# Kernel tuning notes

Hardware: AMD Instinct MI355X
Metric: run time of the kernel (lower is better)

## Reference

```python
import jax, jax.numpy as jnp
import numpy as np

B, T, D = 64, 2048, 256


def setup_inputs() -> dict:
    key = jax.random.key(0)
    k0, k1, k2, k3 = jax.random.split(key, 4)
    x0 = jax.random.normal(k0, (B, D), dtype=jnp.float32)
    I = jax.random.normal(k1, (B, T, D), dtype=jnp.float32)
    # Scale transition matrix so spectral norm < 1 (stable 2048-step recurrence),
    # mimicking eW = expm((W - I)*dt/tau) which is contractive for stable W.
    eW = jax.random.normal(k2, (D, D), dtype=jnp.float32) * (0.9 / np.sqrt(D))
    W_inv_eW = jax.random.normal(k3, (D, D), dtype=jnp.float32) * (1.0 / np.sqrt(D))
    return {"x0": x0, "I": I, "eW": eW, "W_inv_eW": W_inv_eW}


def reference(x0, I, eW, W_inv_eW):
    # x[:,0]=x0; x[:,t] = x[:,t-1] @ eW.T + I[:,t-1] @ W_inv_eW.T
    u = jnp.einsum('btd,sd->bts', I, W_inv_eW)  # [B, T, D], precompute input drive

    def step(x, u_t):
        x_new = x @ eW.T + u_t  # [B, D]
        return x_new, x_new

    # only u[:, :T-1] is consumed (x[:,t] uses I[:,t-1])
    _, xs = jax.lax.scan(step, x0, jnp.swapaxes(u[:, :-1], 0, 1))  # xs: [T-1, B, D]
    x = jnp.concatenate([x0[:, None, :], jnp.swapaxes(xs, 0, 1)], axis=1)  # [B, T, D]
    return x
```

## Files before the change

### kernel.cpp

```cpp
#include <hip/hip_runtime.h>
#include <stdint.h>
#include <stddef.h>


#define BATCH 64
#define TLEN 2048
#define DDIM 256
#define CHUNK 32
#define NCHUNK 64

typedef __attribute__((ext_vector_type(8))) short short8;
typedef __attribute__((ext_vector_type(4))) float f32x4;
typedef __attribute__((ext_vector_type(16))) float f32x16;

#define MFMA16(a, b, c) __builtin_amdgcn_mfma_f32_16x16x32_bf16((a), (b), (c), 0, 0, 0)
#define MFMA32(a, b, c) __builtin_amdgcn_mfma_f32_32x32x16_bf16((a), (b), (c), 0, 0, 0)
#define PIN8(x) asm volatile("" : "+v"(x))

__device__ __forceinline__ uint16_t f2bf(float f) {
  union { float f; uint32_t u; } v; v.f = f;
  return (uint16_t)((v.u + 0x7fffu + ((v.u >> 16) & 1u)) >> 16);
}
__device__ __forceinline__ float bf2f(uint16_t h) {
  union { uint32_t u; float f; } v; v.u = ((uint32_t)h) << 16;
  return v.f;
}

__device__ __forceinline__ void split8(const float* fv, short8& hi, short8& lo) {
#pragma unroll
  for (int j = 0; j < 8; ++j) {
    uint16_t hb = f2bf(fv[j]);
    hi[j] = (short)hb;
    lo[j] = (short)f2bf(fv[j] - bf2f(hb));
  }
}

__device__ __forceinline__ uint32_t swz(int row) {
  return ((uint32_t)((row & 7) << 4)) ^ ((uint32_t)(((row >> 3) & 1) << 7));
}
__device__ __forceinline__ uint32_t swz32(int row) {
  return ((uint32_t)((row & 7) << 4)) ^ ((uint32_t)(((row >> 3) & 3) << 7));
}

__device__ __forceinline__ void wg_barrier() {
  __builtin_amdgcn_sched_barrier(0);
  asm volatile("s_waitcnt lgkmcnt(0)" ::: "memory");
  __builtin_amdgcn_s_barrier();
  asm volatile("" ::: "memory");
  __builtin_amdgcn_sched_barrier(0);
}

#define WS_M1F    (0)
#define WS_M1_HI  (256 * 1024)
#define WS_M1_LO  (384 * 1024)
#define WS_M2F    (512 * 1024)
#define WS_M2_HI  (768 * 1024)
#define WS_M2_LO  (896 * 1024)
#define WS_M3F    (1024 * 1024)
#define WS_M3_HI  (1280 * 1024)
#define WS_M3_LO  (1408 * 1024)
#define WS_S      (2560 * 1024)

__global__ __launch_bounds__(512, 1) void k_u(const float* __restrict__ I,
                                              const float* __restrict__ Wi,
                                              float* __restrict__ out) {
  const int tid = threadIdx.x;
  const int w = tid >> 6, l = tid & 63, l31 = l & 31, half = l >> 5;
  const int ns = w * 32;
  __shared__ __align__(16) uint16_t sIh[2][8192];
  __shared__ __align__(16) uint16_t sIl[2][8192];

  short8 bh[16], bl[16];
#pragma unroll
  for (int ks = 0; ks < 16; ++ks) {
    const float* wp = Wi + (size_t)(ns + l31) * 256 + ks * 16 + half * 8;
    f32x4 f0 = *reinterpret_cast<const f32x4*>(wp);
    f32x4 f1 = *reinterpret_cast<const f32x4*>(wp + 4);
    float fv[8] = {f0[0], f0[1], f0[2], f0[3], f1[0], f1[1], f1[2], f1[3]};
    split8(fv, bh[ks], bl[ks]);
    PIN8(bh[ks]);
    PIN8(bl[ks]);
  }

  const int srow = tid >> 4;
  const int sc0 = (tid & 15) * 16;
  const uint32_t wb0 = ((uint32_t)(srow * 512 + sc0 * 2)) ^ swz32(srow);
  const uint32_t wb1 = ((uint32_t)(srow * 512 + sc0 * 2 + 16)) ^ swz32(srow);

  const int b0 = blockIdx.x >> 6;
  const int tt = blockIdx.x & 63;
  const bool edge = (tt == 63);
  const size_t S4 = (size_t)4 * TLEN * DDIM;
  const float* Ip = I + ((size_t)b0 * TLEN + tt * 32 + srow) * DDIM + sc0;
  float* Op = out + ((size_t)b0 * TLEN + tt * 32 + 1) * DDIM + ns + l31;

  uint32_t ro[16];
#pragma unroll
  for (int ks = 0; ks < 16; ++ks)
    ro[ks] = ((uint32_t)(l31 * 512 + ks * 32 + half * 16)) ^ swz32(l31);
  int rowoff[16];
#pragma unroll
  for (int r = 0; r < 16; ++r)
    rowoff[r] = ((r & 3) + 8 * (r >> 2) + 4 * half) * DDIM;

  f32x4 ra[4], rb[4];
  auto loadI = [&](int it, f32x4 (&dst)[4]) {
    const float* src = Ip + (size_t)it * S4;
#pragma unroll
    for (int j = 0; j < 4; ++j)
      dst[j] = *reinterpret_cast<const f32x4*>(src + j * 4);
  };

  auto do_tile = [&](int it, f32x4 (&cur)[4], int q, bool pre) {
    short8 hi[2], lo[2];
#pragma unroll
    for (int h2 = 0; h2 < 2; ++h2) {
      float fv[8] = {cur[h2 * 2][0], cur[h2 * 2][1], cur[h2 * 2][2], cur[h2 * 2][3],
                     cur[h2 * 2 + 1][0], cur[h2 * 2 + 1][1], cur[h2 * 2 + 1][2], cur[h2 * 2 + 1][3]};
      split8(fv, hi[h2], lo[h2]);
    }
    if (pre) loadI(it + 2, cur);
    *reinterpret_cast<short8*>(reinterpret_cast<char*>(sIh[q]) + wb0) = hi[0];
    *reinterpret_cast<short8*>(reinterpret_cast<char*>(sIh[q]) + wb1) = hi[1];
    *reinterpret_cast<short8*>(reinterpret_cast<char*>(sIl[q]) + wb0) = lo[0];
    *reinterpret_cast<short8*>(reinterpret_cast<char*>(sIl[q]) + wb1) = lo[1];
    wg_barrier();
    f32x16 acc;
#pragma unroll
    for (int j = 0; j < 16; ++j) acc[j] = 0.f;
    __builtin_amdgcn_s_setprio(1);
#pragma unroll
    for (int ks = 0; ks < 16; ++ks) {
      short8 ih = *reinterpret_cast<const short8*>((const char*)sIh[q] + ro[ks]);
      short8 il = *reinterpret_cast<const short8*>((const char*)sIl[q] + ro[ks]);
      acc = MFMA32(ih, bh[ks], acc);
      acc = MFMA32(il, bh[ks], acc);
      acc = MFMA32(ih, bl[ks], acc);
    }
    __builtin_amdgcn_s_setprio(0);
    float* ob = Op + (size_t)it * S4;
    if (!edge) {
#pragma unroll
      for (int r = 0; r < 16; ++r) ob[rowoff[r]] = acc[r];
    } else {
#pragma unroll
      for (int r = 0; r < 16; ++r)
        if (rowoff[r] < 31 * DDIM) ob[rowoff[r]] = acc[r];
    }
  };

  loadI(0, ra);
  loadI(1, rb);
#pragma unroll 1
  for (int it = 0; it < 16; it += 2) {
    do_tile(it, ra, 0, it + 2 < 16);
    do_tile(it + 1, rb, 1, it + 3 < 16);
  }
}

__global__ __launch_bounds__(1024) void k_scan(const int pass,
                                               const float* __restrict__ eW,
                                               float* __restrict__ xu,
                                               const float* __restrict__ x0,
                                               float* __restrict__ S,
                                               const uint16_t* __restrict__ M1h,
                                               const uint16_t* __restrict__ M1l,
                                               const uint16_t* __restrict__ M2h,
                                               const uint16_t* __restrict__ M2l) {
  const int tid = threadIdx.x;
  const int w = tid >> 6, l = tid & 63, l15 = l & 15, quad = l >> 4;
  const int ns = w * 16;
  const int c = blockIdx.x >> 2;
  const int rg = blockIdx.x & 3;
  __shared__ __align__(16) uint16_t sh[2][4096];
  __shared__ __align__(16) uint16_t sl[2][4096];

  const int t0 = c * CHUNK;
  const int nsteps = (t0 + CHUNK <= TLEN - 1) ? CHUNK : (TLEN - 1 - t0);

  const size_t TD = (size_t)TLEN * DDIM;
  const float* ubase = xu + (size_t)(rg * 16 + quad * 4) * TD + (size_t)(t0 + 1) * DDIM + ns + l15;
  const float* pL = ubase;
  float* pS = const_cast<float*>(ubase);

  float u0[4], u1[4], u2[4], u3[4], fin[4];
#pragma unroll
  for (int j = 0; j < 4; ++j) { u0[j] = 0.f; u1[j] = 0.f; u2[j] = 0.f; u3[j] = 0.f; fin[j] = 0.f; }

  auto issue_at = [&](float (&dst)[4]) {
#pragma unroll
    for (int r = 0; r < 4; ++r) dst[r] = pL[(size_t)r * TD];
  };
  issue_at(u0); pL += DDIM;
  issue_at(u1); pL += DDIM;
  issue_at(u2); pL += DDIM;
  issue_at(u3); pL += DDIM;

  short8 fAh[8], fAl[8];
#pragma unroll
  for (int ks = 0; ks < 8; ++ks) {
    const float* ap = eW + (size_t)(ns + l15) * 256 + ks * 32 + quad * 8;
    f32x4 f0 = *reinterpret_cast<const f32x4*>(ap);
    f32x4 f1 = *reinterpret_cast<const f32x4*>(ap + 4);
    float fv[8] = {f0[0], f0[1], f0[2], f0[3], f1[0], f1[1], f1[2], f1[3]};
    split8(fv, fAh[ks], fAl[ks]);
    PIN8(fAh[ks]);
    PIN8(fAl[ks]);
  }

  uint32_t ro[8];
#pragma unroll
  for (int ks = 0; ks < 8; ++ks)
    ro[ks] = ((uint32_t)(l15 * 512 + ks * 64 + quad * 16)) ^ swz(l15);
  uint32_t wo[4];
#pragma unroll
  for (int r = 0; r < 4; ++r) {
    int row = quad * 4 + r;
    wo[r] = ((uint32_t)(row * 512 + (ns + l15) * 2)) ^ swz(row);
  }

  if (pass == 1) {
    for (int i = tid; i < 4096; i += 1024) {
      int row = i >> 8, k = i & 255;
      uint32_t byte = ((uint32_t)(row * 512 + k * 2)) ^ swz(row);
      *(uint16_t*)((char*)sh[0] + byte) = 0;
      *(uint16_t*)((char*)sl[0] + byte) = 0;
    }
  } else {
    f32x4 yacc;
    {
      const float* Tc = (c == 0) ? x0 : (S + (size_t)(c - 1) * 64 * 256);
#pragma unroll
      for (int r = 0; r < 4; ++r)
        yacc[r] = Tc[(size_t)(rg * 16 + quad * 4 + r) * 256 + ns + l15];
    }
#pragma unroll 1
    for (int j = 1; j <= 2; ++j) {
      int k = c - j;
      if (k < 0) break;
      const float* Tp = (k == 0) ? x0 : (S + (size_t)(k - 1) * 64 * 256);
      const uint16_t* Bh = (j == 1) ? M1h : M2h;
      const uint16_t* Bl = (j == 1) ? M1l : M2l;
#pragma unroll
      for (int ks = 0; ks < 8; ++ks) {
        const float* ap = Tp + (size_t)(rg * 16 + l15) * 256 + ks * 32 + quad * 8;
        f32x4 f0 = *reinterpret_cast<const f32x4*>(ap);
        f32x4 f1 = *reinterpret_cast<const f32x4*>(ap + 4);
        float fv[8] = {f0[0], f0[1], f0[2], f0[3], f1[0], f1[1], f1[2], f1[3]};
        short8 ah, al8;
        split8(fv, ah, al8);
        const int off = (ns + l15) * 256 + ks * 32 + quad * 8;
        short8 bhf = *reinterpret_cast<const short8*>(Bh + off);
        short8 blf = *reinterpret_cast<const short8*>(Bl + off);
        yacc = MFMA16(ah, bhf, yacc);
        yacc = MFMA16(al8, bhf, yacc);
        yacc = MFMA16(ah, blf, yacc);
      }
    }
#pragma unroll
    for (int r = 0; r < 4; ++r) {
      int row = quad * 4 + r, col = ns + l15;
      float v = yacc[r];
      if (c == 0) xu[((size_t)(rg * 16 + row) * TLEN) * DDIM + col] = v;
      uint16_t hb = f2bf(v);
      uint16_t lb = f2bf(v - bf2f(hb));
      *(uint16_t*)((char*)sh[0] + wo[r]) = hb;
      *(uint16_t*)((char*)sl[0] + wo[r]) = lb;
    }
  }
  wg_barrier();

  int p = 0;
  auto step = [&](int i, float (&ucur)[4]) {
    f32x4 acc = {0.f, 0.f, 0.f, 0.f};
    __builtin_amdgcn_s_setprio(1);
#pragma unroll
    for (int ks = 0; ks < 8; ++ks) {
      short8 xh = *reinterpret_cast<const short8*>((const char*)sh[p] + ro[ks]);
      short8 xl = *reinterpret_cast<const short8*>((const char*)sl[p] + ro[ks]);
      acc = MFMA16(xh, fAh[ks], acc);
      acc = MFMA16(xl, fAh[ks], acc);
      acc = MFMA16(xh, fAl[ks], acc);
    }
    __builtin_amdgcn_s_setprio(0);
#pragma unroll
    for (int r = 0; r < 4; ++r) fin[r] = acc[r] + ucur[r];
    if (i + 4 <= nsteps) issue_at(ucur);
    pL += DDIM;
    if (pass == 2) {
#pragma unroll
      for (int r = 0; r < 4; ++r) pS[(size_t)r * TD] = fin[r];
    }
    pS += DDIM;
    if (i < nsteps) {
#pragma unroll
      for (int r = 0; r < 4; ++r) {
        float v = fin[r];
        uint16_t hb = f2bf(v);
        uint16_t lb = f2bf(v - bf2f(hb));
        *(uint16_t*)((char*)sh[p ^ 1] + wo[r]) = hb;
        *(uint16_t*)((char*)sl[p ^ 1] + wo[r]) = lb;
      }
      wg_barrier();
      p ^= 1;
    }
  };

  int i = 1;
  for (; i + 3 <= nsteps; i += 4) {
    step(i, u0);
    step(i + 1, u1);
    step(i + 2, u2);
    step(i + 3, u3);
  }
  if (i <= nsteps) { step(i, u0); ++i; }
  if (i <= nsteps) { step(i, u1); ++i; }
  if (i <= nsteps) { step(i, u2); ++i; }

  if (pass == 1) {
#pragma unroll
    for (int r = 0; r < 4; ++r) {
      int row = quad * 4 + r, col = ns + l15;
      S[((size_t)c * 64 + rg * 16 + row) * DDIM + col] = fin[r];
    }
  }
}

__global__ __launch_bounds__(512) void k_mm256A(const float* __restrict__ eW,
                                                float* __restrict__ Of,
                                                uint16_t* __restrict__ Oh,
                                                uint16_t* __restrict__ Ol) {
  const int mf = blockIdx.x;
  const int tid = threadIdx.x;
  const int w = tid >> 6, l = tid & 63, l15 = l & 15, quad = l >> 4;
  const int ns = w * 32;
  f32x4 acc[2];
  acc[0] = {0.f, 0.f, 0.f, 0.f};
  acc[1] = {0.f, 0.f, 0.f, 0.f};

#pragma unroll
  for (int ks = 0; ks < 8; ++ks) {
    float fv[8];
#pragma unroll
    for (int j = 0; j < 8; ++j)
      fv[j] = eW[(size_t)(ks * 32 + quad * 8 + j) * 256 + mf * 16 + l15];
    short8 ah, al8;
    split8(fv, ah, al8);
#pragma unroll
    for (int nf = 0; nf < 2; ++nf) {
      const float* bp = eW + (size_t)(ns + nf * 16 + l15) * 256 + ks * 32 + quad * 8;
      f32x4 b0 = *reinterpret_cast<const f32x4*>(bp);
      f32x4 b1 = *reinterpret_cast<const f32x4*>(bp + 4);
      float bv[8] = {b0[0], b0[1], b0[2], b0[3], b1[0], b1[1], b1[2], b1[3]};
      short8 bhf, blf;
      split8(bv, bhf, blf);
      acc[nf] = MFMA16(ah, bhf, acc[nf]);
      acc[nf] = MFMA16(al8, bhf, acc[nf]);
      acc[nf] = MFMA16(ah, blf, acc[nf]);
    }
  }
#pragma unroll
  for (int nf = 0; nf < 2; ++nf)
#pragma unroll
    for (int r = 0; r < 4; ++r) {
      int row = mf * 16 + quad * 4 + r;
      int col = ns + nf * 16 + l15;
      float v = acc[nf][r];
      Of[(size_t)row * 256 + col] = v;
      uint16_t hb = f2bf(v);
      Oh[(size_t)col * 256 + row] = hb;
      Ol[(size_t)col * 256 + row] = f2bf(v - bf2f(hb));
    }
}

__global__ __launch_bounds__(512) void k_mm256(const float* __restrict__ Af,
                                               const uint16_t* __restrict__ Bh,
                                               const uint16_t* __restrict__ Bl,
                                               float* __restrict__ Of,
                                               uint16_t* __restrict__ Oh,
                                               uint16_t* __restrict__ Ol) {
  const int mf = blockIdx.x;
  const int tid = threadIdx.x;
  const int w = tid >> 6, l = tid & 63, l15 = l & 15, quad = l >> 4;
  const int ns = w * 32;
  f32x4 acc[2];
  acc[0] = {0.f, 0.f, 0.f, 0.f};
  acc[1] = {0.f, 0.f, 0.f, 0.f};

#pragma unroll
  for (int ks = 0; ks < 8; ++ks) {
    const float* ap = Af + (size_t)(mf * 16 + l15) * 256 + ks * 32 + quad * 8;
    f32x4 f0 = *reinterpret_cast<const f32x4*>(ap);
    f32x4 f1 = *reinterpret_cast<const f32x4*>(ap + 4);
    float fv[8] = {f0[0], f0[1], f0[2], f0[3], f1[0], f1[1], f1[2], f1[3]};
    short8 ah, al8;
    split8(fv, ah, al8);
#pragma unroll
    for (int nf = 0; nf < 2; ++nf) {
      const int off = (ns + nf * 16 + l15) * 256 + ks * 32 + quad * 8;
      short8 bhf = *reinterpret_cast<const short8*>(Bh + off);
      short8 blf = *reinterpret_cast<const short8*>(Bl + off);
      acc[nf] = MFMA16(ah, bhf, acc[nf]);
      acc[nf] = MFMA16(al8, bhf, acc[nf]);
      acc[nf] = MFMA16(ah, blf, acc[nf]);
    }
  }
#pragma unroll
  for (int nf = 0; nf < 2; ++nf)
#pragma unroll
    for (int r = 0; r < 4; ++r) {
      int row = mf * 16 + quad * 4 + r;
      int col = ns + nf * 16 + l15;
      float v = acc[nf][r];
      Of[(size_t)row * 256 + col] = v;
      uint16_t hb = f2bf(v);
      Oh[(size_t)col * 256 + row] = hb;
      Ol[(size_t)col * 256 + row] = f2bf(v - bf2f(hb));
    }
}

extern "C" void kernel_launch(void* const* d_in, const int* in_sizes, int n_in,
                              void* d_out, int out_size, void* d_ws, size_t ws_size,
                              hipStream_t stream) {
  (void)in_sizes; (void)n_in; (void)out_size; (void)ws_size;
  const float* x0 = (const float*)d_in[0];
  const float* I  = (const float*)d_in[1];
  const float* eW = (const float*)d_in[2];
  const float* Wi = (const float*)d_in[3];
  float* out = (float*)d_out;
  char* ws = (char*)d_ws;

  float*    M1f = (float*)(ws + WS_M1F);
  uint16_t* M1h = (uint16_t*)(ws + WS_M1_HI);
  uint16_t* M1l = (uint16_t*)(ws + WS_M1_LO);
  float*    M2f = (float*)(ws + WS_M2F);
  uint16_t* M2h = (uint16_t*)(ws + WS_M2_HI);
  uint16_t* M2l = (uint16_t*)(ws + WS_M2_LO);
  float*    M3f = (float*)(ws + WS_M3F);
  uint16_t* M3h = (uint16_t*)(ws + WS_M3_HI);
  uint16_t* M3l = (uint16_t*)(ws + WS_M3_LO);
  float*    S   = (float*)(ws + WS_S);

  k_u<<<256, 512, 0, stream>>>(I, Wi, out);
  k_mm256A<<<16, 512, 0, stream>>>(eW, M3f, M3h, M3l);
  k_mm256<<<16, 512, 0, stream>>>(M3f, M3h, M3l, M2f, M2h, M2l);
  k_mm256<<<16, 512, 0, stream>>>(M2f, M2h, M2l, M3f, M3h, M3l);
  k_mm256<<<16, 512, 0, stream>>>(M3f, M3h, M3l, M2f, M2h, M2l);
  k_mm256<<<16, 512, 0, stream>>>(M2f, M2h, M2l, M1f, M1h, M1l);
  k_mm256<<<16, 512, 0, stream>>>(M1f, M1h, M1l, M2f, M2h, M2l);
  k_scan<<<256, 1024, 0, stream>>>(1, eW, out, x0, S, M1h, M1l, M2h, M2l);
  k_scan<<<256, 1024, 0, stream>>>(2, eW, out, x0, S, M1h, M1l, M2h, M2l);
}
```

Measured before the change: 293.8 us.

## Halve scan chunk length, use 512-thread blocks and three-chunk carry propagation

Chunk length drops from 32 to 16 steps, doubling the number of chunks to 128 and the grid to 512 blocks of 512 threads. Each wave now computes two 16-column N-fragments, so eW is held in registers twice per wave. The carry fixup pass uses powers M1, M2, M3 of eW (eW^16, eW^32, eW^48) to combine the three previous chunk end states, and the matrix-power launch sequence is rearranged to produce them. The aim is to shorten the serial dependency chain per block and fill more CUs, at the cost of extra fixup MFMAs and higher register pressure.

Result: slower. 776.7 us (+164.4%).

```diff
diff --git a/kernel.cpp b/kernel.cpp
--- a/kernel.cpp
+++ b/kernel.cpp
@@ -6,8 +6,8 @@
 #define BATCH 64
 #define TLEN 2048
 #define DDIM 256
-#define CHUNK 32
-#define NCHUNK 64
+#define CHUNK 16
+#define NCHUNK 128
 
 typedef __attribute__((ext_vector_type(8))) short short8;
 typedef __attribute__((ext_vector_type(4))) float f32x4;
@@ -158,18 +158,20 @@
   }
 }
 
-__global__ __launch_bounds__(1024) void k_scan(const int pass,
-                                               const float* __restrict__ eW,
-                                               float* __restrict__ xu,
-                                               const float* __restrict__ x0,
-                                               float* __restrict__ S,
-                                               const uint16_t* __restrict__ M1h,
-                                               const uint16_t* __restrict__ M1l,
-                                               const uint16_t* __restrict__ M2h,
-                                               const uint16_t* __restrict__ M2l) {
+__global__ __launch_bounds__(512, 4) void k_scan(const int pass,
+                                                 const float* __restrict__ eW,
+                                                 float* __restrict__ xu,
+                                                 const float* __restrict__ x0,
+                                                 float* __restrict__ S,
+                                                 const uint16_t* __restrict__ M1h,
+                                                 const uint16_t* __restrict__ M1l,
+                                                 const uint16_t* __restrict__ M2h,
+                                                 const uint16_t* __restrict__ M2l,
+                                                 const uint16_t* __restrict__ M3h,
+                                                 const uint16_t* __restrict__ M3l) {
   const int tid = threadIdx.x;
   const int w = tid >> 6, l = tid & 63, l15 = l & 15, quad = l >> 4;
-  const int ns = w * 16;
+  const int ns = w * 32;
   const int c = blockIdx.x >> 2;
   const int rg = blockIdx.x & 3;
   __shared__ __align__(16) uint16_t sh[2][4096];
@@ -178,69 +180,63 @@
   const int t0 = c * CHUNK;
   const int nsteps = (t0 + CHUNK <= TLEN - 1) ? CHUNK : (TLEN - 1 - t0);
 
-  const size_t TD = (size_t)TLEN * DDIM;
-  const float* ubase = xu + (size_t)(rg * 16 + quad * 4) * TD + (size_t)(t0 + 1) * DDIM + ns + l15;
-  const float* pL = ubase;
-  float* pS = const_cast<float*>(ubase);
-
-  float u0[4], u1[4], u2[4], u3[4], fin[4];
-#pragma unroll
-  for (int j = 0; j < 4; ++j) { u0[j] = 0.f; u1[j] = 0.f; u2[j] = 0.f; u3[j] = 0.f; fin[j] = 0.f; }
-
-  auto issue_at = [&](float (&dst)[4]) {
-#pragma unroll
-    for (int r = 0; r < 4; ++r) dst[r] = pL[(size_t)r * TD];
+  float u0[8], u1[8], u2[8], u3[8], fin[8];
+#pragma unroll
+  for (int j = 0; j < 8; ++j) { u0[j] = 0.f; u1[j] = 0.f; u2[j] = 0.f; u3[j] = 0.f; fin[j] = 0.f; }
+
+  auto issue_u = [&](int i, float (&dst)[8]) {
+    if (i > nsteps) return;
+#pragma unroll
+    for (int nf = 0; nf < 2; ++nf)
+#pragma unroll
+      for (int r = 0; r < 4; ++r) {
+        int b = rg * 16 + quad * 4 + r;
+        dst[nf * 4 + r] = xu[((size_t)b * TLEN + t0 + i) * DDIM + ns + nf * 16 + l15];
+      }
   };
-  issue_at(u0); pL += DDIM;
-  issue_at(u1); pL += DDIM;
-  issue_at(u2); pL += DDIM;
-  issue_at(u3); pL += DDIM;
-
-  short8 fAh[8], fAl[8];
-#pragma unroll
-  for (int ks = 0; ks < 8; ++ks) {
-    const float* ap = eW + (size_t)(ns + l15) * 256 + ks * 32 + quad * 8;
-    f32x4 f0 = *reinterpret_cast<const f32x4*>(ap);
-    f32x4 f1 = *reinterpret_cast<const f32x4*>(ap + 4);
-    float fv[8] = {f0[0], f0[1], f0[2], f0[3], f1[0], f1[1], f1[2], f1[3]};
-    split8(fv, fAh[ks], fAl[ks]);
-    PIN8(fAh[ks]);
-    PIN8(fAl[ks]);
-  }
-
-  uint32_t ro[8];
-#pragma unroll
-  for (int ks = 0; ks < 8; ++ks)
-    ro[ks] = ((uint32_t)(l15 * 512 + ks * 64 + quad * 16)) ^ swz(l15);
-  uint32_t wo[4];
-#pragma unroll
-  for (int r = 0; r < 4; ++r) {
-    int row = quad * 4 + r;
-    wo[r] = ((uint32_t)(row * 512 + (ns + l15) * 2)) ^ swz(row);
-  }
+  issue_u(1, u0);
+  issue_u(2, u1);
+  issue_u(3, u2);
+  issue_u(4, u3);
+
+  short8 fAh[2][8], fAl[2][8];
+#pragma unroll
+  for (int nf = 0; nf < 2; ++nf)
+#pragma unroll
+    for (int ks = 0; ks < 8; ++ks) {
+      const float* ap = eW + (size_t)(ns + nf * 16 + l15) * 256 + ks * 32 + quad * 8;
+      f32x4 f0 = *reinterpret_cast<const f32x4*>(ap);
+      f32x4 f1 = *reinterpret_cast<const f32x4*>(ap + 4);
+      float fv[8] = {f0[0], f0[1], f0[2], f0[3], f1[0], f1[1], f1[2], f1[3]};
+      split8(fv, fAh[nf][ks], fAl[nf][ks]);
+      PIN8(fAh[nf][ks]);
+      PIN8(fAl[nf][ks]);
+    }
 
   if (pass == 1) {
-    for (int i = tid; i < 4096; i += 1024) {
+    for (int i = tid; i < 4096; i += 512) {
       int row = i >> 8, k = i & 255;
       uint32_t byte = ((uint32_t)(row * 512 + k * 2)) ^ swz(row);
       *(uint16_t*)((char*)sh[0] + byte) = 0;
       *(uint16_t*)((char*)sl[0] + byte) = 0;
     }
   } else {
-    f32x4 yacc;
+    f32x4 yacc[2];
     {
       const float* Tc = (c == 0) ? x0 : (S + (size_t)(c - 1) * 64 * 256);
 #pragma unroll
-      for (int r = 0; r < 4; ++r)
-        yacc[r] = Tc[(size_t)(rg * 16 + quad * 4 + r) * 256 + ns + l15];
+      for (int nf = 0; nf < 2; ++nf)
+#pragma unroll
+        for (int r = 0; r < 4; ++r)
+          yacc[nf][r] = Tc[(size_t)(rg * 16 + quad * 4 + r) * 256 + ns + nf * 16 + l15];
     }
 #pragma unroll 1
-    for (int j = 1; j <= 2; ++j) {
+    for (int j = 1; j <= 3; ++j) {
       int k = c - j;
       if (k < 0) break;
       const float* Tp = (k == 0) ? x0 : (S + (size_t)(k - 1) * 64 * 256);
-      const uint16_t* Bh = (j == 1) ? M1h : M2h;
-      const uint16_t* Bl = (j == 1) ? M1l : M2l;
+      const uint16_t* Bh = (j == 1) ? M1h : (j == 2) ? M2h : M3h;
+      const uint16_t* Bl = (j == 1) ? M1l : (j == 2) ? M2l : M3l;
 #pragma unroll
       for (int ks = 0; ks < 8; ++ks) {
         const float* ap = Tp + (size_t)(rg * 16 + l15) * 256 + ks * 32 + quad * 8;
@@ -249,58 +245,78 @@
         float fv[8] = {f0[0], f0[1], f0[2], f0[3], f1[0], f1[1], f1[2], f1[3]};
         short8 ah, al8;
         split8(fv, ah, al8);
-        const int off = (ns + l15) * 256 + ks * 32 + quad * 8;
-        short8 bhf = *reinterpret_cast<const short8*>(Bh + off);
-        short8 blf = *reinterpret_cast<const short8*>(Bl + off);
-        yacc = MFMA16(ah, bhf, yacc);
-        yacc = MFMA16(al8, bhf, yacc);
-        yacc = MFMA16(ah, blf, yacc);
+#pragma unroll
+        for (int nf = 0; nf < 2; ++nf) {
+          const int off = (ns + nf * 16 + l15) * 256 + ks * 32 + quad * 8;
+          short8 bhf = *reinterpret_cast<const short8*>(Bh + off);
+          short8 blf = *reinterpret_cast<const short8*>(Bl + off);
+          yacc[nf] = MFMA16(ah, bhf, yacc[nf]);
+          yacc[nf] = MFMA16(al8, bhf, yacc[nf]);
+          yacc[nf] = MFMA16(ah, blf, yacc[nf]);
+        }
       }
     }
 #pragma unroll
-    for (int r = 0; r < 4; ++r) {
-      int row = quad * 4 + r, col = ns + l15;
-      float v = yacc[r];
-      if (c == 0) xu[((size_t)(rg * 16 + row) * TLEN) * DDIM + col] = v;
-      uint16_t hb = f2bf(v);
-      uint16_t lb = f2bf(v - bf2f(hb));
-      *(uint16_t*)((char*)sh[0] + wo[r]) = hb;
-      *(uint16_t*)((char*)sl[0] + wo[r]) = lb;
-    }
-  }
-  wg_barrier();
-
-  int p = 0;
-  auto step = [&](int i, float (&ucur)[4]) {
-    f32x4 acc = {0.f, 0.f, 0.f, 0.f};
-    __builtin_amdgcn_s_setprio(1);
-#pragma unroll
-    for (int ks = 0; ks < 8; ++ks) {
-      short8 xh = *reinterpret_cast<const short8*>((const char*)sh[p] + ro[ks]);
-      short8 xl = *reinterpret_cast<const short8*>((const char*)sl[p] + ro[ks]);
-      acc = MFMA16(xh, fAh[ks], acc);
-      acc = MFMA16(xl, fAh[ks], acc);
-      acc = MFMA16(xh, fAl[ks], acc);
-    }
-    __builtin_amdgcn_s_setprio(0);
-#pragma unroll
-    for (int r = 0; r < 4; ++r) fin[r] = acc[r] + ucur[r];
-    if (i + 4 <= nsteps) issue_at(ucur);
-    pL += DDIM;
-    if (pass == 2) {
-#pragma unroll
-      for (int r = 0; r < 4; ++r) pS[(size_t)r * TD] = fin[r];
-    }
-    pS += DDIM;
-    if (i < nsteps) {
+    for (int nf = 0; nf < 2; ++nf)
 #pragma unroll
       for (int r = 0; r < 4; ++r) {
-        float v = fin[r];
+        int row = quad * 4 + r, col = ns + nf * 16 + l15;
+        float v = yacc[nf][r];
+        if (c == 0) xu[((size_t)(rg * 16 + row) * TLEN) * DDIM + col] = v;
         uint16_t hb = f2bf(v);
         uint16_t lb = f2bf(v - bf2f(hb));
-        *(uint16_t*)((char*)sh[p ^ 1] + wo[r]) = hb;
-        *(uint16_t*)((char*)sl[p ^ 1] + wo[r]) = lb;
+        uint32_t byte = ((uint32_t)(row * 512 + col * 2)) ^ swz(row);
+        *(uint16_t*)((char*)sh[0] + byte) = hb;
+        *(uint16_t*)((char*)sl[0] + byte) = lb;
       }
+  }
+  wg_barrier();
+
+  int p = 0;
+  auto step = [&](int i, float (&ucur)[8]) {
+    f32x4 acc0 = {0.f, 0.f, 0.f, 0.f}, acc1 = {0.f, 0.f, 0.f, 0.f};
+    __builtin_amdgcn_s_setprio(1);
+#pragma unroll
+    for (int ks = 0; ks < 8; ++ks) {
+      uint32_t byte = ((uint32_t)(l15 * 512 + ks * 64 + quad * 16)) ^ swz(l15);
+      short8 xh = *reinterpret_cast<const short8*>((const char*)sh[p] + byte);
+      short8 xl = *reinterpret_cast<const short8*>((const char*)sl[p] + byte);
+      acc0 = MFMA16(xh, fAh[0][ks], acc0);
+      acc0 = MFMA16(xl, fAh[0][ks], acc0);
+      acc0 = MFMA16(xh, fAl[0][ks], acc0);
+      acc1 = MFMA16(xh, fAh[1][ks], acc1);
+      acc1 = MFMA16(xl, fAh[1][ks], acc1);
+      acc1 = MFMA16(xh, fAl[1][ks], acc1);
+    }
+    __builtin_amdgcn_s_setprio(0);
+#pragma unroll
+    for (int nf = 0; nf < 2; ++nf)
+#pragma unroll
+      for (int r = 0; r < 4; ++r)
+        fin[nf * 4 + r] = (nf ? acc1[r] : acc0[r]) + ucur[nf * 4 + r];
+    issue_u(i + 4, ucur);
+    if (pass == 2) {
+#pragma unroll
+      for (int nf = 0; nf < 2; ++nf)
+#pragma unroll
+        for (int r = 0; r < 4; ++r) {
+          int b = rg * 16 + quad * 4 + r;
+          xu[((size_t)b * TLEN + t0 + i) * DDIM + ns + nf * 16 + l15] = fin[nf * 4 + r];
+        }
+    }
+    if (i < nsteps) {
+#pragma unroll
+      for (int nf = 0; nf < 2; ++nf)
+#pragma unroll
+        for (int r = 0; r < 4; ++r) {
+          int row = quad * 4 + r, col = ns + nf * 16 + l15;
+          float v = fin[nf * 4 + r];
+          uint16_t hb = f2bf(v);
+          uint16_t lb = f2bf(v - bf2f(hb));
+          uint32_t byte = ((uint32_t)(row * 512 + col * 2)) ^ swz(row);
+          *(uint16_t*)((char*)sh[p ^ 1] + byte) = hb;
+          *(uint16_t*)((char*)sl[p ^ 1] + byte) = lb;
+        }
       wg_barrier();
       p ^= 1;
     }
@@ -319,10 +335,12 @@
 
   if (pass == 1) {
 #pragma unroll
-    for (int r = 0; r < 4; ++r) {
-      int row = quad * 4 + r, col = ns + l15;
-      S[((size_t)c * 64 + rg * 16 + row) * DDIM + col] = fin[r];
-    }
+    for (int nf = 0; nf < 2; ++nf)
+#pragma unroll
+      for (int r = 0; r < 4; ++r) {
+        int row = quad * 4 + r, col = ns + nf * 16 + l15;
+        S[((size_t)c * 64 + rg * 16 + row) * DDIM + col] = fin[nf * 4 + r];
+      }
   }
 }
 
@@ -445,9 +463,11 @@
   k_mm256A<<<16, 512, 0, stream>>>(eW, M3f, M3h, M3l);
   k_mm256<<<16, 512, 0, stream>>>(M3f, M3h, M3l, M2f, M2h, M2l);
   k_mm256<<<16, 512, 0, stream>>>(M2f, M2h, M2l, M3f, M3h, M3l);
-  k_mm256<<<16, 512, 0, stream>>>(M3f, M3h, M3l, M2f, M2h, M2l);
-  k_mm256<<<16, 512, 0, stream>>>(M2f, M2h, M2l, M1f, M1h, M1l);
+  k_mm256<<<16, 512, 0, stream>>>(M3f, M3h, M3l, M1f, M1h, M1l);
   k_mm256<<<16, 512, 0, stream>>>(M1f, M1h, M1l, M2f, M2h, M2l);
-  k_scan<<<256, 1024, 0, stream>>>(1, eW, out, x0, S, M1h, M1l, M2h, M2l);
-  k_scan<<<256, 1024, 0, stream>>>(2, eW, out, x0, S, M1h, M1l, M2h, M2l);
-}
+  k_mm256<<<16, 512, 0, stream>>>(M2f, M1h, M1l, M3f, M3h, M3l);
+  k_scan<<<512, 512, 0, stream>>>(1, eW, out, x0, S,
+                                  M1h, M1l, M2h, M2l, M3h, M3l);
+  k_scan<<<512, 512, 0, stream>>>(2, eW, out, x0, S,
+                                  M1h, M1l, M2h, M2l, M3h, M3l);
+}
```
